# Performance work log

Measured on AMD Instinct MI355X. Metric: run time of the kernel, lower is better.

## Reference

```python
import jax, jax.numpy as jnp
import numpy as np

B, L, D, S = 4, 4096, 1024, 16
EPS = 1e-5  # nn.LayerNorm default


def setup_inputs() -> dict:
    key = jax.random.key(0)
    ks = jax.random.split(key, 8)
    s = 0.02
    return {
        "x_seq": jax.random.normal(ks[0], (B, L, D), jnp.float32),
        "h_prev": jnp.zeros((B, S), jnp.float32),
        "gamma": jnp.ones((D,), jnp.float32),
        "beta": jnp.zeros((D,), jnp.float32),
        "W_in": jax.random.normal(ks[1], (D, D), jnp.float32) * s,
        "b_in": jnp.zeros((D,), jnp.float32),
        "W_A": jax.random.normal(ks[2], (D, S), jnp.float32) * s,
        "b_A": jnp.zeros((S,), jnp.float32),
        "W_B": jax.random.normal(ks[3], (D, S), jnp.float32) * s,
        "b_B": jnp.zeros((S,), jnp.float32),
        "W_C": jax.random.normal(ks[4], (D, S), jnp.float32) * s,
        "b_C": jnp.zeros((S,), jnp.float32),
        "W_dt": jax.random.normal(ks[5], (D, 1), jnp.float32) * s,
        "b_dt": jnp.zeros((1,), jnp.float32),
        "W_out": jax.random.normal(ks[6], (D, D), jnp.float32) * s,
        "b_out": jnp.zeros((D,), jnp.float32),
    }


def _layernorm(x, gamma, beta):
    mu = jnp.mean(x, axis=-1, keepdims=True)
    var = jnp.mean(jnp.square(x - mu), axis=-1, keepdims=True)
    return (x - mu) * jax.lax.rsqrt(var + EPS) * gamma + beta


def reference(x_seq, h_prev, gamma, beta, W_in, b_in, W_A, b_A, W_B, b_B,
              W_C, b_C, W_dt, b_dt, W_out, b_out):
    # pre-scan projections (all batched over (B, L))
    x = _layernorm(x_seq, gamma, beta)
    x = jax.nn.silu(x @ W_in + b_in)                    # (B, L, D)
    log_A = -jax.nn.softplus(x @ W_A + b_A)             # (B, L, S)
    B_t = x @ W_B + b_B                                 # (B, L, S)
    C_t = x @ W_C + b_C                                 # (B, L, S)
    dt = jax.nn.softplus(x @ W_dt + b_dt)               # (B, L, 1)
    A_disc = jnp.exp(log_A * dt)                        # (B, L, S)
    u = jnp.mean(x, axis=-1, keepdims=True)             # (B, L, 1)
    Bu = (B_t * dt) * u                                 # (B, L, S)

    # selective scan: h_t = A_t * h_{t-1} + Bu_t  over time axis
    def step(h, inp):
        a_t, bu_t = inp
        h = a_t * h + bu_t
        return h, h

    h_final, hs = jax.lax.scan(
        step, h_prev,
        (jnp.swapaxes(A_disc, 0, 1), jnp.swapaxes(Bu, 0, 1)))
    hs = jnp.swapaxes(hs, 0, 1)                         # (B, L, S)

    y = jnp.sum(C_t * hs, axis=-1, keepdims=True)       # (B, L, 1)
    y_seq = (x * y) @ W_out + b_out + x_seq             # (B, L, D)
    return y_seq, h_final
```

## Files before the change

### kernel.cpp

```cpp
#include <hip/hip_runtime.h>

typedef unsigned short u16;
typedef unsigned int u32;
typedef __attribute__((ext_vector_type(8))) short short8;
typedef __attribute__((ext_vector_type(4))) float f32x4;

#define B_ 4
#define L_ 4096
#define D_ 1024
#define S_ 16
#define M_ (B_ * L_)
#define NBG 64
#define LC 64

__device__ __forceinline__ float b2f(u16 h) {
    unsigned u = ((unsigned)h) << 16;
    return __builtin_bit_cast(float, u);
}
__device__ __forceinline__ u16 f2b(float f) {
    unsigned u = __builtin_bit_cast(unsigned, f);
    u += 0x7fffu + ((u >> 16) & 1u);
    return (u16)(u >> 16);
}
__device__ __forceinline__ float softplus_f(float z) {
    return z > 20.f ? z : log1pf(__expf(z));
}
__device__ __forceinline__ void gload16(const u16* g, const u16* l) {
    __builtin_amdgcn_global_load_lds(
        (const __attribute__((address_space(1))) u32*)g,
        (__attribute__((address_space(3))) u32*)l, 16, 0, 0);
}

__global__ __launch_bounds__(256) void ln_prep_kernel(
    const float* __restrict__ x, const float* __restrict__ gamma,
    const float* __restrict__ beta, u16* __restrict__ xout,
    const float* __restrict__ W0, u16* __restrict__ Wt0,
    const float* __restrict__ W1, u16* __restrict__ Wt1,
    const float* __restrict__ WA, const float* __restrict__ WB,
    const float* __restrict__ WC, const float* __restrict__ Wdt,
    u16* __restrict__ Wp) {
    int blk = blockIdx.x, tid = threadIdx.x;
    if (blk < M_) {
        int row = blk;
        const float4 v = *(const float4*)&x[(size_t)row * D_ + tid * 4];
        float s = v.x + v.y + v.z + v.w;
        float q = v.x * v.x + v.y * v.y + v.z * v.z + v.w * v.w;
        for (int o = 32; o > 0; o >>= 1) { s += __shfl_down(s, o); q += __shfl_down(q, o); }
        __shared__ float ss[4], qq[4];
        int w = tid >> 6, lane = tid & 63;
        if (lane == 0) { ss[w] = s; qq[w] = q; }
        __syncthreads();
        if (tid == 0) {
            float S = ss[0] + ss[1] + ss[2] + ss[3];
            float Q = qq[0] + qq[1] + qq[2] + qq[3];
            float mu = S * (1.f / D_);
            float var = Q * (1.f / D_) - mu * mu;
            ss[0] = mu; qq[0] = rsqrtf(var + 1e-5f);
        }
        __syncthreads();
        float mu = ss[0], rs = qq[0];
        const float4 gv = *(const float4*)&gamma[tid * 4];
        const float4 bv = *(const float4*)&beta[tid * 4];
        ushort4 o4;
        o4.x = f2b((v.x - mu) * rs * gv.x + bv.x);
        o4.y = f2b((v.y - mu) * rs * gv.y + bv.y);
        o4.z = f2b((v.z - mu) * rs * gv.z + bv.z);
        o4.w = f2b((v.w - mu) * rs * gv.w + bv.w);
        *(ushort4*)&xout[(size_t)row * D_ + tid * 4] = o4;
    } else if (blk < M_ + 2048) {
        int b = blk - M_;
        const float* W = (b >> 10) ? W1 : W0;
        u16* Wt = (b >> 10) ? Wt1 : Wt0;
        int by = (b >> 5) & 31, bx = b & 31;
        int xx = tid & 31, ty = tid >> 5;
        __shared__ float t[32][33];
        for (int j = ty; j < 32; j += 8)
            t[j][xx] = W[(size_t)(by * 32 + j) * D_ + bx * 32 + xx];
        __syncthreads();
        for (int j = ty; j < 32; j += 8)
            Wt[(size_t)(bx * 32 + j) * D_ + by * 32 + xx] = f2b(t[xx][j]);
    } else {
        int idx = (blk - M_ - 2048) * 256 + tid;
        int s = idx >> 10, k = idx & 1023;
        float v;
        if (s < 16)       v = WA[k * 16 + s];
        else if (s < 32)  v = WB[k * 16 + (s - 16)];
        else if (s < 48)  v = WC[k * 16 + (s - 32)];
        else if (s == 48) v = Wdt[k];
        else if (s == 49) v = 1.0f / 1024.0f;
        else              v = 0.f;
        Wp[idx] = f2b(v);
    }
}

template <int EPI>
__global__ __launch_bounds__(512, 1) void gemm256(
    const u16* __restrict__ A, const u16* __restrict__ Bt,
    const float* __restrict__ bias, const float* __restrict__ resid,
    const float* __restrict__ yrow,
    u16* __restrict__ outB, float* __restrict__ outF,
    int M, int N, int K, int nTileN) {
    __shared__ u16 sm[65536];
    const int TILES = K >> 6;

    int nwg = gridDim.x;
    int bid = blockIdx.x;
    int swz = (bid & 7) * (nwg >> 3) + (bid >> 3);
    int bx = swz % nTileN, by = swz / nTileN;
    int rowBase = by * 256, colBase = bx * 256;

    int tid = threadIdx.x;
    int lane = tid & 63, w = tid >> 6;
    int wr = w >> 2, wc = w & 3;
    int lr = lane & 15, lg = lane >> 4;
    const unsigned woff = (unsigned)((lr * 32 + lg * 8) ^ ((lr & 8) ? 16 : 0));

    int sub = w;
    int pos = sub >> 1;
    int kblk = sub & 1;
    int r = lane >> 2;
    int chunk = (lane & 3) ^ ((r & 8) ? 2 : 0);
    int rowoff = (pos & 1) * 16 + (pos >> 1) * 128;
    const u16* gAs = A  + (size_t)(rowBase + rowoff + r) * K + kblk * 32 + chunk * 8;
    const u16* gBs = Bt + (size_t)(colBase + rowoff + r) * K + kblk * 32 + chunk * 8;
    const unsigned subb = (unsigned)sub * 512u;

#define STAGEPAIR(tau, p)                                                        \
    do {                                                                         \
        unsigned _bb = (unsigned)((tau) & 1) * 32768u;                           \
        size_t _go = (size_t)(p) * 32 * K + (size_t)(tau) * 64;                  \
        gload16(gBs + _go, &sm[_bb + 16384u + (unsigned)(p) * 4096u + subb]);    \
        gload16(gAs + _go, &sm[_bb + (unsigned)(p) * 4096u + subb]);             \
    } while (0)

    f32x4 acc[8][4] = {};

    STAGEPAIR(0, 0); STAGEPAIR(0, 1); STAGEPAIR(0, 2); STAGEPAIR(0, 3);
    if (TILES > 1) { STAGEPAIR(1, 0); STAGEPAIR(1, 1); STAGEPAIR(1, 2); }
    asm volatile("s_waitcnt vmcnt(6)" ::: "memory");
    __builtin_amdgcn_s_barrier();

    for (int t = 0; t < TILES; ++t) {
        const unsigned bb = (unsigned)(t & 1) * 32768u;
        short8 bfr[4][2], afr[2][2];
        if (t + 1 < TILES) STAGEPAIR(t + 1, 3);
#pragma unroll
        for (int n = 0; n < 4; n++) {
            int rb = wc * 4 + n;
            unsigned bo = bb + 16384u + (unsigned)(((rb & 7) >> 1)) * 4096u
                        + (unsigned)(((rb & 1) + ((rb >> 3) << 1)) << 1) * 512u + woff;
            bfr[n][0] = *(const short8*)&sm[bo];
            bfr[n][1] = *(const short8*)&sm[bo + 512u];
        }
#pragma unroll
        for (int dm = 0; dm < 2; dm++) {
            unsigned ao = bb + (unsigned)((dm + (wr << 1)) << 1) * 512u + woff;
            afr[dm][0] = *(const short8*)&sm[ao];
            afr[dm][1] = *(const short8*)&sm[ao + 512u];
        }
        __builtin_amdgcn_s_barrier();
        __builtin_amdgcn_s_setprio(1);
#pragma unroll
        for (int dm = 0; dm < 2; dm++)
#pragma unroll
            for (int n = 0; n < 4; n++)
#pragma unroll
                for (int ks = 0; ks < 2; ks++)
                    acc[dm][n] = __builtin_amdgcn_mfma_f32_16x16x32_bf16(
                        afr[dm][ks], bfr[n][ks], acc[dm][n], 0, 0, 0);
        __builtin_amdgcn_s_setprio(0);
        __builtin_amdgcn_s_barrier();
#pragma unroll
        for (int q = 1; q < 4; q++) {
            if (t + 2 < TILES) STAGEPAIR(t + 2, q - 1);
#pragma unroll
            for (int dm = 0; dm < 2; dm++) {
                int m = q * 2 + dm;
                unsigned ao = bb + (unsigned)q * 4096u
                            + (unsigned)(((m & 1) + (wr << 1)) << 1) * 512u + woff;
                afr[dm][0] = *(const short8*)&sm[ao];
                afr[dm][1] = *(const short8*)&sm[ao + 512u];
            }
            __builtin_amdgcn_s_barrier();
            __builtin_amdgcn_s_setprio(1);
#pragma unroll
            for (int dm = 0; dm < 2; dm++)
#pragma unroll
                for (int n = 0; n < 4; n++)
#pragma unroll
                    for (int ks = 0; ks < 2; ks++)
                        acc[q * 2 + dm][n] = __builtin_amdgcn_mfma_f32_16x16x32_bf16(
                            afr[dm][ks], bfr[n][ks], acc[q * 2 + dm][n], 0, 0, 0);
            __builtin_amdgcn_s_setprio(0);
            if (q == 3) {
                if (t + 2 < TILES)      asm volatile("s_waitcnt vmcnt(6)" ::: "memory");
                else if (t + 1 < TILES) asm volatile("s_waitcnt vmcnt(0)" ::: "memory");
            }
            __builtin_amdgcn_s_barrier();
        }
    }
#undef STAGEPAIR

    if (EPI == 1) {
        float bcol[4];
#pragma unroll
        for (int n = 0; n < 4; n++) bcol[n] = bias[colBase + wc * 64 + n * 16 + lr];
#pragma unroll
        for (int m = 0; m < 8; m++)
#pragma unroll
            for (int n = 0; n < 4; n++)
#pragma unroll
                for (int j = 0; j < 4; j++) {
                    int row = wr * 128 + m * 16 + lg * 4 + j;
                    int col = wc * 64 + n * 16 + lr;
                    float v = acc[m][n][j] + bcol[n];
                    v = v / (1.f + __expf(-v));
                    int cbs = (col >> 4) ^ lg;
                    sm[row * 256 + cbs * 16 + (col & 15)] = f2b(v);
                }
        __syncthreads();
        int rr = tid >> 1, half = tid & 1;
        u16* gout = outB + (size_t)(rowBase + rr) * N + colBase;
#pragma unroll
        for (int q = 0; q < 8; q++) {
            int cb = half * 8 + q;
            int cbs = cb ^ ((rr >> 2) & 3);
            *(uint4*)&gout[cb * 16] = *(const uint4*)&sm[rr * 256 + cbs * 16];
        }
    } else {
        float bcol[4];
#pragma unroll
        for (int n = 0; n < 4; n++) bcol[n] = bias[colBase + wc * 64 + n * 16 + lr];
#pragma unroll
        for (int m = 0; m < 8; m++) {
            float yr[4];
#pragma unroll
            for (int j = 0; j < 4; j++)
                yr[j] = yrow[rowBase + wr * 128 + m * 16 + lg * 4 + j];
#pragma unroll
            for (int n = 0; n < 4; n++)
#pragma unroll
                for (int j = 0; j < 4; j++) {
                    int row = rowBase + wr * 128 + m * 16 + lg * 4 + j;
                    int col = colBase + wc * 64 + n * 16 + lr;
                    size_t o = (size_t)row * N + col;
                    outF[o] = acc[m][n][j] * yr[j] + bcol[n] + resid[o];
                }
        }
    }
}

__global__ __launch_bounds__(256) void proj_kernel(
    const u16* __restrict__ X, const u16* __restrict__ Wp,
    const float* __restrict__ bA, const float* __restrict__ bB,
    const float* __restrict__ bC, const float* __restrict__ bdt,
    float* __restrict__ Ad, float* __restrict__ Bu, float* __restrict__ Ct,
    float* __restrict__ Pb, float* __restrict__ Qb) {
    __shared__ u16 Xs[2][64][32];
    __shared__ u16 Ws[2][64][32];
    __shared__ float Psh[64][17], Qsh[64][17];
    int rowBase = blockIdx.x * 64;
    int tid = threadIdx.x, lane = tid & 63, w = tid >> 6;
    int lr = lane & 15, lg = lane >> 4;
    f32x4 acc[4] = {};
    const int sr = lane >> 2, sc = (lane & 3) * 8;
    const u16* gX = &X[(size_t)(rowBase + w * 16 + sr) * 1024 + sc];
    const u16* gW = &Wp[(size_t)(w * 16 + sr) * 1024 + sc];

#define PSTAGE(d, k0)                              \
    do {                                           \
        gload16(gX + (k0), &Xs[d][w * 16][0]);     \
        gload16(gW + (k0), &Ws[d][w * 16][0]);     \
    } while (0)

    PSTAGE(0, 0);
    __syncthreads();
    int cur = 0;
    for (int k0 = 0; k0 < 1024; k0 += 32) {
        if (k0 + 32 < 1024) PSTAGE(cur ^ 1, k0 + 32);
        short8 a = *(const short8*)&Xs[cur][w * 16 + lr][lg * 8];
#pragma unroll
        for (int n = 0; n < 4; n++) {
            short8 b = *(const short8*)&Ws[cur][n * 16 + lr][lg * 8];
            acc[n] = __builtin_amdgcn_mfma_f32_16x16x32_bf16(a, b, acc[n], 0, 0, 0);
        }
        __syncthreads();
        cur ^= 1;
    }
#undef PSTAGE
    float bdt0 = bdt[0];
#pragma unroll
    for (int j = 0; j < 4; j++) {
        int rl = w * 16 + lg * 4 + j;
        int row = rowBase + rl;
        float dtr = __shfl(acc[3][j], lg * 16 + 0, 64);
        float uv  = __shfl(acc[3][j], lg * 16 + 1, 64);
        float dt = softplus_f(dtr + bdt0);
        float zA = acc[0][j] + bA[lr];
        float zB = acc[1][j] + bB[lr];
        float zC = acc[2][j] + bC[lr];
        size_t o = (size_t)row * 16 + lr;
        float adv = __expf(-dt * softplus_f(zA));
        float buv = zB * dt * uv;
        Ad[o] = adv;
        Bu[o] = buv;
        Ct[o] = zC;
        Psh[rl][lr] = adv;
        Qsh[rl][lr] = buv;
    }
    __syncthreads();
    if (tid < 16) {
        float P = 1.f, Q = 0.f;
        for (int rr = 0; rr < 64; rr++) {
            float pa = Psh[rr][tid];
            P = pa * P;
            Q = pa * Q + Qsh[rr][tid];
        }
        int o = blockIdx.x * S_ + tid;
        Pb[o] = P; Qb[o] = Q;
    }
}

__global__ __launch_bounds__(1024) void scan_part3(
    const float* __restrict__ Ad, const float* __restrict__ Bu,
    const float* __restrict__ Ct, const float* __restrict__ Pb,
    const float* __restrict__ Qb, const float* __restrict__ hprev,
    float* __restrict__ y, float* __restrict__ hfinal) {
    int b = blockIdx.x >> 6, g = blockIdx.x & 63;
    int tid = threadIdx.x;
    int s = tid & 15, c = tid >> 4;
    size_t idx = ((size_t)b * L_ + g * LC + c) * S_ + s;
    float a = Ad[idx], bu = Bu[idx];
    __shared__ float Ps[16][64], Qs[16][64], Hin[16][65];
    Ps[s][c] = a; Qs[s][c] = bu;
    __syncthreads();
    if (tid < 16) {
        float h = hprev[b * S_ + tid];
        for (int gg = 0; gg < g; gg++) {
            int o = (b * NBG + gg) * S_ + tid;
            h = Pb[o] * h + Qb[o];
        }
        for (int cc = 0; cc < 64; cc++) {
            Hin[tid][cc] = h;
            h = Ps[tid][cc] * h + Qs[tid][cc];
        }
        if (g == NBG - 1) hfinal[b * S_ + tid] = h;
    }
    __syncthreads();
    float h = a * Hin[s][c] + bu;
    float p = Ct[idx] * h;
    p += __shfl_xor(p, 1);
    p += __shfl_xor(p, 2);
    p += __shfl_xor(p, 4);
    p += __shfl_xor(p, 8);
    if (s == 0) y[(size_t)b * L_ + g * LC + c] = p;
}

extern "C" void kernel_launch(void* const* d_in, const int* in_sizes, int n_in,
                              void* d_out, int out_size, void* d_ws, size_t ws_size,
                              hipStream_t stream) {
    const float* x_seq  = (const float*)d_in[0];
    const float* h_prev = (const float*)d_in[1];
    const float* gamma  = (const float*)d_in[2];
    const float* beta   = (const float*)d_in[3];
    const float* W_in   = (const float*)d_in[4];
    const float* b_in   = (const float*)d_in[5];
    const float* W_A    = (const float*)d_in[6];
    const float* b_A    = (const float*)d_in[7];
    const float* W_B    = (const float*)d_in[8];
    const float* b_B    = (const float*)d_in[9];
    const float* W_C    = (const float*)d_in[10];
    const float* b_C    = (const float*)d_in[11];
    const float* W_dt   = (const float*)d_in[12];
    const float* b_dt   = (const float*)d_in[13];
    const float* W_out  = (const float*)d_in[14];
    const float* b_out  = (const float*)d_in[15];

    char* ws = (char*)d_ws;
    u16*   x_ln   = (u16*)(ws + 0);
    u16*   x      = (u16*)(ws + 33554432);
    u16*   Wt_in  = (u16*)(ws + 67108864);
    u16*   Wt_out = (u16*)(ws + 69206016);
    u16*   Wp     = (u16*)(ws + 71303168);
    float* Ad     = (float*)(ws + 71434240);
    float* Bu     = (float*)(ws + 72482816);
    float* Ct     = (float*)(ws + 73531392);
    float* yv     = (float*)(ws + 74579968);
    float* Pb     = (float*)(ws + 74645504);
    float* Qb     = (float*)(ws + 74661888);
    float* out    = (float*)d_out;

    ln_prep_kernel<<<M_ + 2048 + 256, 256, 0, stream>>>(
        x_seq, gamma, beta, x_ln,
        W_in, Wt_in, W_out, Wt_out, W_A, W_B, W_C, W_dt, Wp);
    gemm256<1><<<(M_ / 256) * (D_ / 256), 512, 0, stream>>>(
        x_ln, Wt_in, b_in, nullptr, nullptr, x, nullptr, M_, D_, D_, D_ / 256);
    proj_kernel<<<M_ / 64, 256, 0, stream>>>(x, Wp, b_A, b_B, b_C, b_dt,
                                             Ad, Bu, Ct, Pb, Qb);
    scan_part3<<<B_ * NBG, 1024, 0, stream>>>(Ad, Bu, Ct, Pb, Qb, h_prev,
                                              yv, out + (size_t)M_ * D_);
    gemm256<2><<<(M_ / 256) * (D_ / 256), 512, 0, stream>>>(
        x, Wt_out, b_out, x_seq, yv, nullptr, out, M_, D_, D_, D_ / 256);
}
```

Before: 152.0 us.

## Fuse projection and chunked scan into one cooperative kernel with grid sync

Merges the small projection GEMM and the chunked selective scan into a single cooperative kernel. Per-chunk A_disc, Bu and C stay in shared memory, and a grid-wide sync separates the chunk summary pass from the carry-propagation pass. This removes the global round-trip of Ad/Bu/Ct and one kernel launch. In exchange it relies on a cooperative launch of 256 blocks and a grid barrier, and the final scan pass now runs in 256 threads with 4 sequential steps each instead of 1024 threads.

```diff
diff --git a/kernel.cpp b/kernel.cpp
--- a/kernel.cpp
+++ b/kernel.cpp
@@ -1,4 +1,7 @@
 #include <hip/hip_runtime.h>
+#include <hip/hip_cooperative_groups.h>
+
+namespace cg = cooperative_groups;
 
 typedef unsigned short u16;
 typedef unsigned int u32;
@@ -250,16 +253,20 @@
     }
 }
 
-__global__ __launch_bounds__(256) void proj_kernel(
+__global__ __launch_bounds__(256) void proj_scan_kernel(
     const u16* __restrict__ X, const u16* __restrict__ Wp,
     const float* __restrict__ bA, const float* __restrict__ bB,
     const float* __restrict__ bC, const float* __restrict__ bdt,
-    float* __restrict__ Ad, float* __restrict__ Bu, float* __restrict__ Ct,
-    float* __restrict__ Pb, float* __restrict__ Qb) {
+    const float* __restrict__ hprev,
+    float* __restrict__ Pb, float* __restrict__ Qb,
+    float* __restrict__ yv, float* __restrict__ hfinal) {
     __shared__ u16 Xs[2][64][32];
     __shared__ u16 Ws[2][64][32];
-    __shared__ float Psh[64][17], Qsh[64][17];
-    int rowBase = blockIdx.x * 64;
+    __shared__ float Ad_l[64][17], Bu_l[64][17], Ct_l[64][17];
+    __shared__ float Hin[16][17];
+    int blk = blockIdx.x;
+    int b = blk >> 6, g = blk & 63;
+    int rowBase = blk * 64;
     int tid = threadIdx.x, lane = tid & 63, w = tid >> 6;
     int lr = lane & 15, lg = lane >> 4;
     f32x4 acc[4] = {};
@@ -281,8 +288,8 @@
         short8 a = *(const short8*)&Xs[cur][w * 16 + lr][lg * 8];
 #pragma unroll
         for (int n = 0; n < 4; n++) {
-            short8 b = *(const short8*)&Ws[cur][n * 16 + lr][lg * 8];
-            acc[n] = __builtin_amdgcn_mfma_f32_16x16x32_bf16(a, b, acc[n], 0, 0, 0);
+            short8 bfr = *(const short8*)&Ws[cur][n * 16 + lr][lg * 8];
+            acc[n] = __builtin_amdgcn_mfma_f32_16x16x32_bf16(a, bfr, acc[n], 0, 0, 0);
         }
         __syncthreads();
         cur ^= 1;
@@ -292,48 +299,32 @@
 #pragma unroll
     for (int j = 0; j < 4; j++) {
         int rl = w * 16 + lg * 4 + j;
-        int row = rowBase + rl;
         float dtr = __shfl(acc[3][j], lg * 16 + 0, 64);
         float uv  = __shfl(acc[3][j], lg * 16 + 1, 64);
         float dt = softplus_f(dtr + bdt0);
         float zA = acc[0][j] + bA[lr];
         float zB = acc[1][j] + bB[lr];
         float zC = acc[2][j] + bC[lr];
-        size_t o = (size_t)row * 16 + lr;
         float adv = __expf(-dt * softplus_f(zA));
         float buv = zB * dt * uv;
-        Ad[o] = adv;
-        Bu[o] = buv;
-        Ct[o] = zC;
-        Psh[rl][lr] = adv;
-        Qsh[rl][lr] = buv;
+        Ad_l[rl][lr] = adv;
+        Bu_l[rl][lr] = buv;
+        Ct_l[rl][lr] = zC;
     }
     __syncthreads();
     if (tid < 16) {
         float P = 1.f, Q = 0.f;
         for (int rr = 0; rr < 64; rr++) {
-            float pa = Psh[rr][tid];
+            float pa = Ad_l[rr][tid];
             P = pa * P;
-            Q = pa * Q + Qsh[rr][tid];
-        }
-        int o = blockIdx.x * S_ + tid;
+            Q = pa * Q + Bu_l[rr][tid];
+        }
+        int o = blk * S_ + tid;
         Pb[o] = P; Qb[o] = Q;
     }
-}
-
-__global__ __launch_bounds__(1024) void scan_part3(
-    const float* __restrict__ Ad, const float* __restrict__ Bu,
-    const float* __restrict__ Ct, const float* __restrict__ Pb,
-    const float* __restrict__ Qb, const float* __restrict__ hprev,
-    float* __restrict__ y, float* __restrict__ hfinal) {
-    int b = blockIdx.x >> 6, g = blockIdx.x & 63;
-    int tid = threadIdx.x;
-    int s = tid & 15, c = tid >> 4;
-    size_t idx = ((size_t)b * L_ + g * LC + c) * S_ + s;
-    float a = Ad[idx], bu = Bu[idx];
-    __shared__ float Ps[16][64], Qs[16][64], Hin[16][65];
-    Ps[s][c] = a; Qs[s][c] = bu;
-    __syncthreads();
+
+    cg::this_grid().sync();
+
     if (tid < 16) {
         float h = hprev[b * S_ + tid];
         for (int gg = 0; gg < g; gg++) {
@@ -341,19 +332,25 @@
             h = Pb[o] * h + Qb[o];
         }
         for (int cc = 0; cc < 64; cc++) {
-            Hin[tid][cc] = h;
-            h = Ps[tid][cc] * h + Qs[tid][cc];
+            if ((cc & 3) == 0) Hin[tid][cc >> 2] = h;
+            h = Ad_l[cc][tid] * h + Bu_l[cc][tid];
         }
         if (g == NBG - 1) hfinal[b * S_ + tid] = h;
     }
     __syncthreads();
-    float h = a * Hin[s][c] + bu;
-    float p = Ct[idx] * h;
-    p += __shfl_xor(p, 1);
-    p += __shfl_xor(p, 2);
-    p += __shfl_xor(p, 4);
-    p += __shfl_xor(p, 8);
-    if (s == 0) y[(size_t)b * L_ + g * LC + c] = p;
+    int s = tid & 15, c = tid >> 4;
+    float h = Hin[s][c];
+#pragma unroll
+    for (int st = 0; st < 4; st++) {
+        int cc = c * 4 + st;
+        h = Ad_l[cc][s] * h + Bu_l[cc][s];
+        float p = Ct_l[cc][s] * h;
+        p += __shfl_xor(p, 1);
+        p += __shfl_xor(p, 2);
+        p += __shfl_xor(p, 4);
+        p += __shfl_xor(p, 8);
+        if (s == 0) yv[(size_t)rowBase + cc] = p;
+    }
 }
 
 extern "C" void kernel_launch(void* const* d_in, const int* in_sizes, int n_in,
@@ -382,23 +379,26 @@
     u16*   Wt_in  = (u16*)(ws + 67108864);
     u16*   Wt_out = (u16*)(ws + 69206016);
     u16*   Wp     = (u16*)(ws + 71303168);
-    float* Ad     = (float*)(ws + 71434240);
-    float* Bu     = (float*)(ws + 72482816);
-    float* Ct     = (float*)(ws + 73531392);
     float* yv     = (float*)(ws + 74579968);
     float* Pb     = (float*)(ws + 74645504);
     float* Qb     = (float*)(ws + 74661888);
     float* out    = (float*)d_out;
+    float* hfin   = out + (size_t)M_ * D_;
 
     ln_prep_kernel<<<M_ + 2048 + 256, 256, 0, stream>>>(
         x_seq, gamma, beta, x_ln,
         W_in, Wt_in, W_out, Wt_out, W_A, W_B, W_C, W_dt, Wp);
     gemm256<1><<<(M_ / 256) * (D_ / 256), 512, 0, stream>>>(
         x_ln, Wt_in, b_in, nullptr, nullptr, x, nullptr, M_, D_, D_, D_ / 256);
-    proj_kernel<<<M_ / 64, 256, 0, stream>>>(x, Wp, b_A, b_B, b_C, b_dt,
-                                             Ad, Bu, Ct, Pb, Qb);
-    scan_part3<<<B_ * NBG, 1024, 0, stream>>>(Ad, Bu, Ct, Pb, Qb, h_prev,
-                                              yv, out + (size_t)M_ * D_);
+    {
+        const u16* xp = x; const u16* wpp = Wp;
+        const float *bAp = b_A, *bBp = b_B, *bCp = b_C, *bdtp = b_dt, *hpp = h_prev;
+        float *Pbp = Pb, *Qbp = Qb, *yvp = yv, *hfp = hfin;
+        void* args[] = { &xp, &wpp, &bAp, &bBp, &bCp, &bdtp, &hpp,
+                         &Pbp, &Qbp, &yvp, &hfp };
+        hipLaunchCooperativeKernel((void*)proj_scan_kernel,
+                                   dim3(B_ * NBG), dim3(256), args, 0, stream);
+    }
     gemm256<2><<<(M_ / 256) * (D_ / 256), 512, 0, stream>>>(
         x, Wt_out, b_out, x_seq, yv, nullptr, out, M_, D_, D_, D_ / 256);
 }
```

New measurement: 178.7 us. 17.5% more time.
